# Kernel tuning notes

Measured on AMD Instinct MI355X. Metric: run time of the kernel, lower is better.

## Reference

```python
import jax, jax.numpy as jnp
import numpy as np

B, W, E, P, H, NH = 2, 512, 2, 8, 1024, 16
D = H // NH  # 64
T = W + E


def _split_heads(x):
    # [..., S, H] -> [..., NH, S, D]
    x = x.reshape(x.shape[:-1] + (NH, D))
    return jnp.swapaxes(x, -2, -3)


def setup_inputs() -> dict:
    key = jax.random.key(0)
    ks = jax.random.split(key, 16)
    s = 0.02
    inp = {
        "word_hidden_states": jax.random.normal(ks[0], (B, W, H), jnp.float32),
        "entity_hidden_states": jax.random.normal(ks[1], (B, P, E, H), jnp.float32),
        "attention_mask": jnp.zeros((B, 1, 1, T), jnp.float32),
        "q_w": jax.random.normal(ks[2], (H, H), jnp.float32) * s,
        "q_b": jnp.zeros((H,), jnp.float32),
        "k_w": jax.random.normal(ks[3], (H, H), jnp.float32) * s,
        "k_b": jnp.zeros((H,), jnp.float32),
        "v_w": jax.random.normal(ks[4], (H, H), jnp.float32) * s,
        "v_b": jnp.zeros((H,), jnp.float32),
        "w2e_w": jax.random.normal(ks[5], (H, H), jnp.float32) * s,
        "w2e_b": jnp.zeros((H,), jnp.float32),
        "e2w_w": jax.random.normal(ks[6], (H, H), jnp.float32) * s,
        "e2w_b": jnp.zeros((H,), jnp.float32),
        "e2e_w": jax.random.normal(ks[7], (H, H), jnp.float32) * s,
        "e2e_b": jnp.zeros((H,), jnp.float32),
    }
    return inp


def reference(word_hidden_states, entity_hidden_states, attention_mask,
              q_w, q_b, k_w, k_b, v_w, v_b,
              w2e_w, w2e_b, e2w_w, e2w_b, e2e_w, e2e_b):
    words = word_hidden_states          # [B, W, H]
    ents = entity_hidden_states         # [B, P, E, H]

    # Queries: words use `query` and `w2e_query`; entities use `e2w_query` and `e2e_query`.
    w2w_q = _split_heads(words @ q_w + q_b)      # [B, NH, W, D]
    w2e_q = _split_heads(words @ w2e_w + w2e_b)  # [B, NH, W, D]
    e2w_q = _split_heads(ents @ e2w_w + e2w_b)   # [B, P, NH, E, D]
    e2e_q = _split_heads(ents @ e2e_w + e2e_b)   # [B, P, NH, E, D]

    # Shared key/value projection on [expanded words ; entities]. Word K/V are
    # identical across pairs (expand), so compute once and broadcast.
    k_word = _split_heads(words @ k_w + k_b)     # [B, NH, W, D]
    k_ent = _split_heads(ents @ k_w + k_b)       # [B, P, NH, E, D]
    v_word = _split_heads(words @ v_w + v_b)     # [B, NH, W, D]
    v_ent = _split_heads(ents @ v_w + v_b)       # [B, P, NH, E, D]

    # Four block score matrices.
    s_w2w = jnp.einsum('bhqd,bhkd->bhqk', w2w_q, k_word)      # [B, NH, W, W]
    s_w2e = jnp.einsum('bhqd,bphkd->bphqk', w2e_q, k_ent)     # [B, P, NH, W, E]
    s_e2w = jnp.einsum('bphqd,bhkd->bphqk', e2w_q, k_word)    # [B, P, NH, E, W]
    s_e2e = jnp.einsum('bphqd,bphkd->bphqk', e2e_q, k_ent)    # [B, P, NH, E, E]

    word_scores = jnp.concatenate(
        [jnp.broadcast_to(s_w2w[:, None], (B, P, NH, W, W)), s_w2e], axis=-1)
    ent_scores = jnp.concatenate([s_e2w, s_e2e], axis=-1)
    scores = jnp.concatenate([word_scores, ent_scores], axis=-2)  # [B, P, NH, T, T]

    scale = jnp.asarray(1.0 / np.sqrt(D), scores.dtype)
    scores = scores * scale + attention_mask[:, None]  # mask broadcasts [B,1,1,1,T]
    probs = jax.nn.softmax(scores, axis=-1)  # dropout: eval mode (deterministic)

    v = jnp.concatenate(
        [jnp.broadcast_to(v_word[:, None], (B, P, NH, W, D)), v_ent], axis=-2)
    ctx = jnp.einsum('bphqk,bphkd->bphqd', probs, v)   # [B, P, NH, T, D]
    ctx = jnp.swapaxes(ctx, -2, -3).reshape(B, P, T, H)

    word_reps = ctx[:, :, :W, :]   # [B, P, W, H]
    ent_reps = ctx[:, :, W:, :]    # [B, P, E, H]
    return (word_reps, ent_reps)
```

## Files before the change

kernel.cpp:

```cpp
#include <hip/hip_runtime.h>
#include <hip/hip_bf16.h>

typedef __attribute__((ext_vector_type(8))) short s16x8;
typedef __attribute__((ext_vector_type(4))) float fx4;
typedef __attribute__((ext_vector_type(4))) unsigned int u32x4;
typedef unsigned short u16;
typedef unsigned int   u32;
typedef unsigned long long u64;

#define DI __device__ __forceinline__


DI float bf2f(u16 x){ u32 u = ((u32)x)<<16; float f; __builtin_memcpy(&f,&u,4); return f; }
DI u16 f2bf(float f){ u32 u; __builtin_memcpy(&u,&f,4); u = (u + 0x7fffu + ((u>>16)&1u))>>16; return (u16)u; }

DI fx4 mfma_16x16x32_bf16(s16x8 a, s16x8 b, fx4 c){
  return __builtin_amdgcn_mfma_f32_16x16x32_bf16(a,b,c,0,0,0);
}

__global__ __launch_bounds__(256) void k_prep(
    const float* __restrict__ s0, const float* __restrict__ s1, const float* __restrict__ s2,
    const float* __restrict__ s3, const float* __restrict__ s4, const float* __restrict__ s5,
    u16* __restrict__ dstbase,
    const float* __restrict__ words, u16* __restrict__ Xbf,
    const float* __restrict__ ents,  u16* __restrict__ Ebf)
{
  __shared__ __align__(16) u16 tile[64][72];
  int bx = blockIdx.x, tid = threadIdx.x;
  if(bx < 1536){
    int z = bx>>8, t = bx&255;
    const float* src = (z==0)?s0:(z==1)?s1:(z==2)?s2:(z==3)?s3:(z==4)?s4:s5;
    u16* dst = dstbase + (u64)z*1048576u;
    int kt = (t&15)*64, nt = (t>>4)*64;
    #pragma unroll
    for(int it=0; it<2; ++it){
      int c = it*256 + tid;
      int r = c>>3, col = (c&7)*8;
      const float* sp = src + (u64)(kt+r)*1024u + nt + col;
      fx4 a = *(const fx4*)sp;
      fx4 b = *(const fx4*)(sp+4);
      u16 o[8];
      o[0]=f2bf(a[0]); o[1]=f2bf(a[1]); o[2]=f2bf(a[2]); o[3]=f2bf(a[3]);
      o[4]=f2bf(b[0]); o[5]=f2bf(b[1]); o[6]=f2bf(b[2]); o[7]=f2bf(b[3]);
      __builtin_memcpy(&tile[r][col], o, 16);
    }
    __syncthreads();
    #pragma unroll
    for(int it=0; it<2; ++it){
      int c = it*256 + tid;
      int nr = c>>3, kc = (c&7)*8;
      u16 tmp[8];
      #pragma unroll
      for(int j=0;j<8;++j) tmp[j] = tile[kc+j][nr];
      u32x4 v; __builtin_memcpy(&v, tmp, 16);
      *(u32x4*)(dst + (u64)(nt+nr)*1024u + kt + kc) = v;
    }
  } else {
    const float* src; u16* dst; int i;
    if(bx < 2048){ src = words; dst = Xbf; i = ((bx-1536)*256 + tid)*8; }
    else         { src = ents;  dst = Ebf; i = ((bx-2048)*256 + tid)*8; }
    fx4 a = *(const fx4*)(src+i);
    fx4 b = *(const fx4*)(src+i+4);
    u16 o[8];
    o[0]=f2bf(a[0]); o[1]=f2bf(a[1]); o[2]=f2bf(a[2]); o[3]=f2bf(a[3]);
    o[4]=f2bf(b[0]); o[5]=f2bf(b[1]); o[6]=f2bf(b[2]); o[7]=f2bf(b[3]);
    u32x4 v; __builtin_memcpy(&v,o,16);
    *(u32x4*)(dst+i)=v;
  }
}

__global__ __launch_bounds__(256) void k_proj(
    const u16* __restrict__ Xbf, const u16* __restrict__ Ebf,
    const u16* __restrict__ wtq, const u16* __restrict__ wtw2e,
    const u16* __restrict__ wtk, const u16* __restrict__ wtv,
    const u16* __restrict__ wte2w, const u16* __restrict__ wte2e,
    const float* __restrict__ qb, const float* __restrict__ w2eb,
    const float* __restrict__ kb, const float* __restrict__ vb,
    const float* __restrict__ e2wb, const float* __restrict__ e2eb,
    u16* __restrict__ Qw, u16* __restrict__ Q2e, u16* __restrict__ Kwp, u16* __restrict__ VwTp,
    u16* __restrict__ Qe2w, u16* __restrict__ Qe2e, u16* __restrict__ Kep, u16* __restrict__ VeTp)
{
  __shared__ __align__(16) u16 XL[128*64];
  __shared__ __align__(16) u16 WL[128*64];
  int tid = threadIdx.x;
  int z = blockIdx.z;
  int wv = tid>>6, lane = tid&63, l15 = lane&15, g = lane>>4;

  if(blockIdx.y < 8){
    const u16* WT  = (z==0)?wtq:(z==1)?wtw2e:(z==2)?wtk:wtv;
    const float* bias = (z==0)?qb :(z==1)?w2eb :(z==2)?kb :vb;
    u16* out       = (z==0)?Qw :(z==1)?Q2e :(z==2)?Kwp :VwTp;
    int nt = blockIdx.x*64;
    int mt = blockIdx.y*128;
    int wr = (wv>>1)*64, wc = (wv&1)*32;
    fx4 acc[4][2] = {};
    u32x4 rx[4], rw[2];
    #pragma unroll
    for(int it=0; it<4; ++it){
      int c = it*256 + tid;
      int r = c>>3, cb = (c&7)*16, scb = cb ^ ((r&7)<<4);
      rx[it] = *(const u32x4*)((const char*)Xbf + ((u64)(mt+r)*1024u)*2u + scb);
    }
    #pragma unroll
    for(int it=0; it<2; ++it){
      int c = it*256 + tid;
      int r = c>>3, cb = (c&7)*16, scb = cb ^ ((r&7)<<4);
      rw[it] = *(const u32x4*)((const char*)WT + ((u64)(nt+r)*1024u)*2u + scb);
    }
    #pragma unroll
    for(int it=0; it<4; ++it) *(u32x4*)((char*)XL + (it*256+tid)*16) = rx[it];
    #pragma unroll
    for(int it=0; it<2; ++it) *(u32x4*)((char*)WL + (it*256+tid)*16) = rw[it];
    __syncthreads();
    for(int t=0; t<16; ++t){
      int kn = (t+1)*64;
      if(t < 15){
        #pragma unroll
        for(int it=0; it<4; ++it){
          int c = it*256 + tid;
          int r = c>>3, cb = (c&7)*16, scb = cb ^ ((r&7)<<4);
          rx[it] = *(const u32x4*)((const char*)Xbf + ((u64)(mt+r)*1024u + kn)*2u + scb);
        }
        #pragma unroll
        for(int it=0; it<2; ++it){
          int c = it*256 + tid;
          int r = c>>3, cb = (c&7)*16, scb = cb ^ ((r&7)<<4);
          rw[it] = *(const u32x4*)((const char*)WT + ((u64)(nt+r)*1024u + kn)*2u + scb);
        }
      }
      #pragma unroll
      for(int ks=0; ks<2; ++ks){
        s16x8 af[4], bfv[2];
        #pragma unroll
        for(int i=0;i<4;++i){
          int ra = wr + i*16 + l15;
          af[i]  = *(const s16x8*)((const char*)XL + ra*128 + ((ks*64 + g*16) ^ ((ra&7)<<4)));
        }
        #pragma unroll
        for(int j=0;j<2;++j){
          int rb = wc + j*16 + l15;
          bfv[j] = *(const s16x8*)((const char*)WL + rb*128 + ((ks*64 + g*16) ^ ((rb&7)<<4)));
        }
        #pragma unroll
        for(int i=0;i<4;++i)
          #pragma unroll
          for(int j=0;j<2;++j)
            acc[i][j] = mfma_16x16x32_bf16(af[i], bfv[j], acc[i][j]);
      }
      __syncthreads();
      if(t < 15){
        #pragma unroll
        for(int it=0; it<4; ++it) *(u32x4*)((char*)XL + (it*256+tid)*16) = rx[it];
        #pragma unroll
        for(int it=0; it<2; ++it) *(u32x4*)((char*)WL + (it*256+tid)*16) = rw[it];
        __syncthreads();
      }
    }
    bool vmode = (z==3);
    #pragma unroll
    for(int j=0;j<2;++j){
      int n = nt + wc + j*16 + l15;
      float bv = bias[n];
      int h = n>>6, d = n&63;
      #pragma unroll
      for(int i=0;i<4;++i){
        #pragma unroll
        for(int q=0;q<4;++q){
          int m = mt + wr + i*16 + g*4 + q;
          int bb = m>>9, wrow = m&511;
          float v = acc[i][j][q] + bv;
          u64 o = vmode ? (((u64)(bb*16+h)*64u + d)*512u + wrow)
                        : (((u64)(bb*16+h)*512u + wrow)*64u + d);
          out[o] = f2bf(v);
        }
      }
    }
  } else {
    if(blockIdx.x >= 8) return;
    const u16* WT  = (z==0)?wte2w:(z==1)?wte2e:(z==2)?wtk:wtv;
    const float* bias = (z==0)?e2wb :(z==1)?e2eb :(z==2)?kb :vb;
    u16* out       = (z==0)?Qe2w :(z==1)?Qe2e :(z==2)?Kep :VeTp;
    int nt = blockIdx.x*128;
    int wc = wv*32;
    fx4 acc[2][2] = {};
    for(int kk=0; kk<1024; kk+=64){
      {
        int r = tid>>3, cb = (tid&7)*16, scb = cb ^ ((r&7)<<4);
        *(u32x4*)((char*)XL + r*128 + cb) =
          *(const u32x4*)((const char*)Ebf + ((u64)r*1024u + kk)*2u + scb);
      }
      #pragma unroll
      for(int it=0; it<4; ++it){
        int c = it*256 + tid;
        int r = c>>3, cb = (c&7)*16, scb = cb ^ ((r&7)<<4);
        *(u32x4*)((char*)WL + r*128 + cb) =
          *(const u32x4*)((const char*)WT + ((u64)(nt+r)*1024u + kk)*2u + scb);
      }
      __syncthreads();
      #pragma unroll
      for(int ks=0; ks<2; ++ks){
        s16x8 af[2], bfv[2];
        #pragma unroll
        for(int i=0;i<2;++i){
          int ra = i*16 + l15;
          af[i]  = *(const s16x8*)((const char*)XL + ra*128 + ((ks*64 + g*16) ^ ((ra&7)<<4)));
          int rb = wc + i*16 + l15;
          bfv[i] = *(const s16x8*)((const char*)WL + rb*128 + ((ks*64 + g*16) ^ ((rb&7)<<4)));
        }
        #pragma unroll
        for(int i=0;i<2;++i)
          #pragma unroll
          for(int j=0;j<2;++j)
            acc[i][j] = mfma_16x16x32_bf16(af[i], bfv[j], acc[i][j]);
      }
      __syncthreads();
    }
    bool vmode = (z==3);
    #pragma unroll
    for(int j=0;j<2;++j){
      int n = nt + wc + j*16 + l15;
      float bv = bias[n];
      int h = n>>6, d = n&63;
      #pragma unroll
      for(int i=0;i<2;++i){
        #pragma unroll
        for(int q=0;q<4;++q){
          int m = i*16 + g*4 + q;
          int bb = m>>4, p = (m>>1)&7, e = m&1;
          float v = acc[i][j][q] + bv;
          u64 base = ((u64)(bb*8+p)*16u + h);
          u64 o = vmode ? ((base*64u + d)*2u + e)
                        : ((base*2u + e)*64u + d);
          out[o] = f2bf(v);
        }
      }
    }
  }
}

__global__ __launch_bounds__(256) void k_attn(
    const u16* __restrict__ Qw,  const u16* __restrict__ Q2e,
    const u16* __restrict__ Kw,  const u16* __restrict__ VwT,
    const u16* __restrict__ Ke,  const u16* __restrict__ VeT,
    const u16* __restrict__ Qe2w, const u16* __restrict__ Qe2e,
    const float* __restrict__ msk, float* __restrict__ outw, float* __restrict__ oute)
{
  const float scale = 0.125f;
  __shared__ __align__(16) u16 KL[128*64];
  __shared__ __align__(16) u16 VtL[64*128];
  __shared__ __align__(16) char UA[4][4608];
  __shared__ __align__(16) float mask_lds[576];
  __shared__ __align__(16) float se_lds[4][16][20];
  __shared__ __align__(16) u16 velds[8*128];
  __shared__ float s_lds[2][516];
  __shared__ float qwl[2][64];
  __shared__ float qel[2][64];
  __shared__ float red[2][8];
  int tid = threadIdx.x;
  int h = blockIdx.y, b = blockIdx.z;
  int wv = tid>>6, lane = tid&63, l15 = lane&15, g = lane>>4;

  if(blockIdx.x < 8){
    int qc = blockIdx.x;
    int q0 = qc*64 + wv*16;

    for(int i=tid;i<576;i+=256) mask_lds[i] = (i<514) ? msk[b*514+i] : 0.f;
    if(tid < 128){
      int p = tid>>4, o = (tid&15)*8;
      *(u32x4*)&velds[p*128 + o] = *(const u32x4*)(VeT + ((u64)(b*8+p)*16u + h)*128u + o);
    }

    const u16* Qrow = Qw + ((u64)(b*16+h)*512u + q0 + l15)*64u;
    s16x8 qf0 = *(const s16x8*)(Qrow + g*8);
    s16x8 qf1 = *(const s16x8*)(Qrow + 32 + g*8);
    const u16* Q2row = Q2e + ((u64)(b*16+h)*512u + q0 + l15)*64u;
    s16x8 q2f0 = *(const s16x8*)(Q2row + g*8);
    s16x8 q2f1 = *(const s16x8*)(Q2row + 32 + g*8);
    const u16* kerow = Ke + ((u64)(b*8+(l15>>1))*16u + h)*128u + (u64)(l15&1)*64u;
    s16x8 keA0 = *(const s16x8*)(kerow + g*8);
    s16x8 keA1 = *(const s16x8*)(kerow + 32 + g*8);
    {
      fx4 se = {0.f,0.f,0.f,0.f};
      se = mfma_16x16x32_bf16(keA0, q2f0, se);
      se = mfma_16x16x32_bf16(keA1, q2f1, se);
      *(fx4*)&se_lds[wv][l15][g*4] = se;
    }

    const char* Kpan = (const char*)(Kw  + (u64)(b*16+h)*512u*64u);
    const char* Vpan = (const char*)(VwT + (u64)(b*16+h)*64u*512u);

    u32x4 rk[4], rv[4];
    auto LOADC = [&](int c){
      #pragma unroll
      for(int it=0;it<4;++it){
        int idx = it*256+tid;
        int r = idx>>3, cb = (idx&7)*16;
        rk[it] = *(const u32x4*)(Kpan + (u64)(c*128+r)*128u + cb);
        int vrr = idx>>4, vcb = (idx&15)*16;
        rv[it] = *(const u32x4*)(Vpan + (u64)vrr*1024u + (u64)c*256u + vcb);
      }
    };
    auto WRITEC = [&](){
      #pragma unroll
      for(int it=0;it<4;++it){
        int idx = it*256+tid;
        int r = idx>>3, cb = (idx&7)*16;
        *(u32x4*)((char*)KL + r*128 + (cb ^ ((r&7)<<4))) = rk[it];
        int vrr = idx>>4, vcb = (idx&15)*16;
        *(u32x4*)((char*)VtL + vrr*256 + (vcb ^ ((vrr&15)<<4))) = rv[it];
      }
    };

    LOADC(0); WRITEC();
    float m_run = -3.0e38f, l_run = 0.f;
    fx4 oacc[4] = {};
    __syncthreads();

    u16 (*PT)[18] = (u16(*)[18])UA[wv];
    for(int c=0;c<4;++c){
      if(c < 3) LOADC(c+1);
      float sv[8][4];
      #pragma unroll
      for(int s=0;s<8;++s){
        int row = s*16 + l15;
        const char* kr = (const char*)KL + row*128;
        int sz = (row&7)<<4;
        s16x8 ka0 = *(const s16x8*)(kr + ((g*16) ^ sz));
        s16x8 ka1 = *(const s16x8*)(kr + ((64 + g*16) ^ sz));
        fx4 st = {0.f,0.f,0.f,0.f};
        st = mfma_16x16x32_bf16(ka0, qf0, st);
        st = mfma_16x16x32_bf16(ka1, qf1, st);
        fx4 mk = *(const fx4*)&mask_lds[c*128 + s*16 + g*4];
        #pragma unroll
        for(int q=0;q<4;++q) sv[s][q] = st[q]*scale + mk[q];
      }
      float cm = -3.0e38f;
      #pragma unroll
      for(int s=0;s<8;++s)
        #pragma unroll
        for(int q=0;q<4;++q) cm = fmaxf(cm, sv[s][q]);
      cm = fmaxf(cm, __shfl_xor(cm, 16, 64));
      cm = fmaxf(cm, __shfl_xor(cm, 32, 64));
      float m_new = fmaxf(m_run, cm);
      float alpha = __expf(m_run - m_new);
      float rs = 0.f;
      #pragma unroll
      for(int s=0;s<8;++s){
        #pragma unroll
        for(int q=0;q<4;++q){
          float e = __expf(sv[s][q] - m_new);
          rs += e;
          PT[s*16 + g*4 + q][l15] = f2bf(e);
        }
      }
      rs += __shfl_xor(rs, 16, 64);
      rs += __shfl_xor(rs, 32, 64);
      l_run = l_run*alpha + rs;
      m_run = m_new;
      #pragma unroll
      for(int t=0;t<4;++t) oacc[t] *= alpha;
      asm volatile("s_waitcnt lgkmcnt(0)" ::: "memory");
      #pragma unroll
      for(int kh=0;kh<4;++kh){
        u16 ptmp[8];
        #pragma unroll
        for(int j=0;j<8;++j) ptmp[j] = PT[kh*32 + g*8 + j][l15];
        s16x8 pbig; __builtin_memcpy(&pbig, ptmp, 16);
        #pragma unroll
        for(int t=0;t<4;++t){
          int vrow = t*16 + l15;
          const char* vr = (const char*)VtL + vrow*256 + ((kh*64 + g*16) ^ ((vrow&15)<<4));
          s16x8 va = *(const s16x8*)vr;
          oacc[t] = mfma_16x16x32_bf16(va, pbig, oacc[t]);
        }
      }
      __syncthreads();
      if(c < 3){ WRITEC(); __syncthreads(); }
    }

    float (*obuf)[68] = (float(*)[68])UA[wv];
    #pragma unroll
    for(int t=0;t<4;++t)
      #pragma unroll
      for(int q=0;q<4;++q)
        obuf[l15][t*16 + g*4 + q] = oacc[t][q];
    asm volatile("s_waitcnt lgkmcnt(0)" ::: "memory");

    int r = lane>>2, cbo = (lane&3)*16;
    fx4 N0 = *(const fx4*)&obuf[r][cbo];
    fx4 N1 = *(const fx4*)&obuf[r][cbo+4];
    fx4 N2 = *(const fx4*)&obuf[r][cbo+8];
    fx4 N3 = *(const fx4*)&obuf[r][cbo+12];
    float m_r = __shfl(m_run, r, 64);
    float l_r = __shfl(l_run, r, 64);
    float mke0 = mask_lds[512], mke1 = mask_lds[513];

    for(int p=0;p<8;++p){
      float s0 = se_lds[wv][r][2*p]  *scale + mke0;
      float s1 = se_lds[wv][r][2*p+1]*scale + mke1;
      float mp = fmaxf(m_r, fmaxf(s0, s1));
      float al = __expf(m_r - mp);
      float p0 = __expf(s0-mp), p1 = __expf(s1-mp);
      float linv = 1.0f/(l_r*al + p0 + p1);
      const u16* vep = velds + p*128 + cbo*2;
      u16 ve[32];
      {
        u32x4 w0 = *(const u32x4*)vep;
        u32x4 w1 = *(const u32x4*)(vep+8);
        u32x4 w2 = *(const u32x4*)(vep+16);
        u32x4 w3 = *(const u32x4*)(vep+24);
        __builtin_memcpy(ve,    &w0, 16);
        __builtin_memcpy(ve+8,  &w1, 16);
        __builtin_memcpy(ve+16, &w2, 16);
        __builtin_memcpy(ve+24, &w3, 16);
      }
      float o[16];
      #pragma unroll
      for(int j=0;j<4;++j){
        o[j]    = (N0[j]*al + p0*bf2f(ve[2*j])      + p1*bf2f(ve[2*j+1]))*linv;
        o[4+j]  = (N1[j]*al + p0*bf2f(ve[8+2*j])    + p1*bf2f(ve[8+2*j+1]))*linv;
        o[8+j]  = (N2[j]*al + p0*bf2f(ve[16+2*j])   + p1*bf2f(ve[16+2*j+1]))*linv;
        o[12+j] = (N3[j]*al + p0*bf2f(ve[24+2*j])   + p1*bf2f(ve[24+2*j+1]))*linv;
      }
      float* og = outw + ((u64)(b*8+p)*512u + q0 + r)*1024u + h*64 + cbo;
      *(fx4*)og      = *(const fx4*)&o[0];
      *(fx4*)(og+4)  = *(const fx4*)&o[4];
      *(fx4*)(og+8)  = *(const fx4*)&o[8];
      *(fx4*)(og+12) = *(const fx4*)&o[12];
    }
  } else {
    int p = blockIdx.x - 8;
    u64 ebase = (u64)(b*8+p)*16u + h;
    if(tid < 128){
      int r = tid>>6, d = tid&63;
      qwl[r][d] = bf2f(Qe2w[(ebase*2 + r)*64 + d]);
      qel[r][d] = bf2f(Qe2e[(ebase*2 + r)*64 + d]);
    }
    __syncthreads();
    const u16* Kpan = Kw + (u64)(b*16+h)*512u*64u;
    for(int k=tid;k<512;k+=256){
      const u16* kr = Kpan + (u64)k*64u;
      float d0=0.f, d1=0.f;
      #pragma unroll
      for(int j=0;j<64;j+=8){
        s16x8 kv = *(const s16x8*)(kr+j);
        #pragma unroll
        for(int x=0;x<8;++x){
          float kf = bf2f((u16)kv[x]);
          d0 += qwl[0][j+x]*kf;
          d1 += qwl[1][j+x]*kf;
        }
      }
      float mk = msk[b*514 + k];
      s_lds[0][k] = d0*0.125f + mk;
      s_lds[1][k] = d1*0.125f + mk;
    }
    if(tid < 4){
      int r = tid>>1, e = tid&1;
      const u16* kr = Ke + (ebase*2 + e)*64;
      float dd = 0.f;
      for(int j=0;j<64;++j) dd += qel[r][j]*bf2f(kr[j]);
      s_lds[r][512+e] = dd*0.125f + msk[b*514 + 512 + e];
    }
    __syncthreads();
    float mx0=-3e38f, mx1=-3e38f;
    for(int k=tid;k<514;k+=256){ mx0=fmaxf(mx0,s_lds[0][k]); mx1=fmaxf(mx1,s_lds[1][k]); }
    #pragma unroll
    for(int off=32; off; off>>=1){
      mx0 = fmaxf(mx0, __shfl_xor(mx0, off, 64));
      mx1 = fmaxf(mx1, __shfl_xor(mx1, off, 64));
    }
    if(lane==0){ red[0][wv]=mx0; red[1][wv]=mx1; }
    __syncthreads();
    float m0 = fmaxf(fmaxf(red[0][0],red[0][1]),fmaxf(red[0][2],red[0][3]));
    float m1 = fmaxf(fmaxf(red[1][0],red[1][1]),fmaxf(red[1][2],red[1][3]));
    float sm0=0.f, sm1=0.f;
    for(int k=tid;k<514;k+=256){
      float e0 = __expf(s_lds[0][k]-m0); s_lds[0][k]=e0; sm0+=e0;
      float e1 = __expf(s_lds[1][k]-m1); s_lds[1][k]=e1; sm1+=e1;
    }
    #pragma unroll
    for(int off=32; off; off>>=1){
      sm0 += __shfl_xor(sm0, off, 64);
      sm1 += __shfl_xor(sm1, off, 64);
    }
    if(lane==0){ red[0][4+wv]=sm0; red[1][4+wv]=sm1; }
    __syncthreads();
    float l0 = red[0][4]+red[0][5]+red[0][6]+red[0][7];
    float l1 = red[1][4]+red[1][5]+red[1][6]+red[1][7];
    if(tid < 128){
      int r = tid>>6, d = tid&63;
      const u16* vr = VwT + ((u64)(b*16+h)*64u + d)*512u;
      float acc = 0.f;
      for(int k=0;k<512;k+=8){
        s16x8 vv = *(const s16x8*)(vr+k);
        #pragma unroll
        for(int x=0;x<8;++x) acc += s_lds[r][k+x]*bf2f((u16)vv[x]);
      }
      const u16* ve = VeT + (ebase*64 + d)*2;
      acc += s_lds[r][512]*bf2f(ve[0]) + s_lds[r][513]*bf2f(ve[1]);
      float val = acc / ((r==0)?l0:l1);
      oute[(((u64)(b*8+p)*2u + r)*1024u + h*64 + d)] = val;
    }
  }
}

extern "C" void kernel_launch(void* const* d_in, const int* in_sizes, int n_in,
                              void* d_out, int out_size, void* d_ws, size_t ws_size,
                              hipStream_t stream)
{
  const float* words = (const float*)d_in[0];
  const float* ents  = (const float*)d_in[1];
  const float* amask = (const float*)d_in[2];
  const float* q_w   = (const float*)d_in[3];
  const float* q_b   = (const float*)d_in[4];
  const float* k_w   = (const float*)d_in[5];
  const float* k_b   = (const float*)d_in[6];
  const float* v_w   = (const float*)d_in[7];
  const float* v_b   = (const float*)d_in[8];
  const float* w2e_w = (const float*)d_in[9];
  const float* w2e_b = (const float*)d_in[10];
  const float* e2w_w = (const float*)d_in[11];
  const float* e2w_b = (const float*)d_in[12];
  const float* e2e_w = (const float*)d_in[13];
  const float* e2e_b = (const float*)d_in[14];

  const size_t MW = 1048576;
  u16* ws16 = (u16*)d_ws;
  if(ws_size < (11*MW + 5*32768)*sizeof(u16)) return;
  u16* WTq   = ws16 + 0*MW;
  u16* WTk   = ws16 + 1*MW;
  u16* WTv   = ws16 + 2*MW;
  u16* WTw2e = ws16 + 3*MW;
  u16* WTe2w = ws16 + 4*MW;
  u16* WTe2e = ws16 + 5*MW;
  u16* Qw    = ws16 + 6*MW;
  u16* Q2e   = ws16 + 7*MW;
  u16* Kwp   = ws16 + 8*MW;
  u16* VwTp  = ws16 + 9*MW;
  u16* Xbf   = ws16 + 10*MW;
  u16* Qe2w  = ws16 + 11*MW;
  u16* Qe2e  = Qe2w + 32768;
  u16* Kep   = Qe2e + 32768;
  u16* VeTp  = Kep + 32768;
  u16* Ebf   = VeTp + 32768;

  dim3 tb(256);
  k_prep<<<dim3(2064), tb, 0, stream>>>(q_w, k_w, v_w, w2e_w, e2w_w, e2e_w, ws16,
                                        words, Xbf, ents, Ebf);
  k_proj<<<dim3(16,9,4), tb, 0, stream>>>(Xbf, Ebf,
      WTq, WTw2e, WTk, WTv, WTe2w, WTe2e,
      q_b, w2e_b, k_b, v_b, e2w_b, e2e_b,
      Qw, Q2e, Kwp, VwTp, Qe2w, Qe2e, Kep, VeTp);
  k_attn<<<dim3(16,16,2), tb, 0, stream>>>(Qw, Q2e, Kwp, VwTp, Kep, VeTp,
      Qe2w, Qe2e, amask, (float*)d_out, (float*)d_out + 8388608u);
}
```

Before: 62.74 us.

## Load V fragments directly from global into registers, drop V LDS staging

The V^T chunk is no longer staged through shared memory. Each wave loads its 16 V fragments straight from global memory into registers for every chunk, and only K stays double-buffered through registers into LDS. This removes the VtL LDS buffer and its write and read traffic. It also adds a launch bound of 3 blocks per CU to raise occupancy. In exchange, every wave in the block reloads the same V data from global/L2 (4x redundancy), and register pressure rises from the 16-vector va array under a tighter register budget.

```diff
diff --git a/kernel.cpp b/kernel.cpp
--- a/kernel.cpp
+++ b/kernel.cpp
@@ -238,7 +238,7 @@
   }
 }
 
-__global__ __launch_bounds__(256) void k_attn(
+__global__ __launch_bounds__(256, 3) void k_attn(
     const u16* __restrict__ Qw,  const u16* __restrict__ Q2e,
     const u16* __restrict__ Kw,  const u16* __restrict__ VwT,
     const u16* __restrict__ Ke,  const u16* __restrict__ VeT,
@@ -247,7 +247,6 @@
 {
   const float scale = 0.125f;
   __shared__ __align__(16) u16 KL[128*64];
-  __shared__ __align__(16) u16 VtL[64*128];
   __shared__ __align__(16) char UA[4][4608];
   __shared__ __align__(16) float mask_lds[576];
   __shared__ __align__(16) float se_lds[4][16][20];
@@ -289,36 +288,31 @@
     const char* Kpan = (const char*)(Kw  + (u64)(b*16+h)*512u*64u);
     const char* Vpan = (const char*)(VwT + (u64)(b*16+h)*64u*512u);
 
-    u32x4 rk[4], rv[4];
-    auto LOADC = [&](int c){
+    u32x4 rk[4];
+    auto LOADK = [&](int c){
       #pragma unroll
       for(int it=0;it<4;++it){
         int idx = it*256+tid;
         int r = idx>>3, cb = (idx&7)*16;
         rk[it] = *(const u32x4*)(Kpan + (u64)(c*128+r)*128u + cb);
-        int vrr = idx>>4, vcb = (idx&15)*16;
-        rv[it] = *(const u32x4*)(Vpan + (u64)vrr*1024u + (u64)c*256u + vcb);
       }
     };
-    auto WRITEC = [&](){
+    auto WRITEK = [&](){
       #pragma unroll
       for(int it=0;it<4;++it){
         int idx = it*256+tid;
         int r = idx>>3, cb = (idx&7)*16;
         *(u32x4*)((char*)KL + r*128 + (cb ^ ((r&7)<<4))) = rk[it];
-        int vrr = idx>>4, vcb = (idx&15)*16;
-        *(u32x4*)((char*)VtL + vrr*256 + (vcb ^ ((vrr&15)<<4))) = rv[it];
       }
     };
 
-    LOADC(0); WRITEC();
+    LOADK(0); WRITEK();
     float m_run = -3.0e38f, l_run = 0.f;
     fx4 oacc[4] = {};
     __syncthreads();
 
     u16 (*PT)[18] = (u16(*)[18])UA[wv];
     for(int c=0;c<4;++c){
-      if(c < 3) LOADC(c+1);
       float sv[8][4];
       #pragma unroll
       for(int s=0;s<8;++s){
@@ -334,6 +328,16 @@
         #pragma unroll
         for(int q=0;q<4;++q) sv[s][q] = st[q]*scale + mk[q];
       }
+      s16x8 va[16];
+      {
+        const char* vbase = Vpan + (u64)c*256u + (u64)l15*1024u + g*16;
+        #pragma unroll
+        for(int t=0;t<4;++t)
+          #pragma unroll
+          for(int kh=0;kh<4;++kh)
+            va[kh*4+t] = *(const s16x8*)(vbase + t*16*1024 + kh*64);
+      }
+      if(c < 3) LOADK(c+1);
       float cm = -3.0e38f;
       #pragma unroll
       for(int s=0;s<8;++s)
@@ -367,15 +371,11 @@
         for(int j=0;j<8;++j) ptmp[j] = PT[kh*32 + g*8 + j][l15];
         s16x8 pbig; __builtin_memcpy(&pbig, ptmp, 16);
         #pragma unroll
-        for(int t=0;t<4;++t){
-          int vrow = t*16 + l15;
-          const char* vr = (const char*)VtL + vrow*256 + ((kh*64 + g*16) ^ ((vrow&15)<<4));
-          s16x8 va = *(const s16x8*)vr;
-          oacc[t] = mfma_16x16x32_bf16(va, pbig, oacc[t]);
-        }
+        for(int t=0;t<4;++t)
+          oacc[t] = mfma_16x16x32_bf16(va[kh*4+t], pbig, oacc[t]);
       }
       __syncthreads();
-      if(c < 3){ WRITEC(); __syncthreads(); }
+      if(c < 3){ WRITEK(); __syncthreads(); }
     }
 
     float (*obuf)[68] = (float(*)[68])UA[wv];
```

New measurement: 70.02 us. +11.6%, slower.
